# Performance work log

Hardware: AMD Instinct MI355X
Metric: run time of the kernel (lower is better)

Reference implementation:

```python
import jax, jax.numpy as jnp
import numpy as np

V, D, NL = 50257, 768, 12
DI, DS, DC, DTR = 1536, 16, 4, 48  # d_inner, d_state, d_conv, dt_rank
B, S = 2, 1024


def _mamba_layer(x, iw, cw, cb, xw, dw, db, Alog, Dp, ow):
    # x: (B,S,D)
    xz = x @ iw.T                      # (B,S,2*DI)
    xin, z = jnp.split(xz, 2, axis=-1)
    # depthwise causal conv over sequence
    xc = jax.lax.conv_general_dilated(
        jnp.transpose(xin, (0, 2, 1)), cw[:, None, :],
        window_strides=(1,), padding=[(DC - 1, 0)],
        feature_group_count=DI, dimension_numbers=('NCL', 'OIL', 'NCL'))
    xin = jax.nn.silu(jnp.transpose(xc, (0, 2, 1)) + cb)  # (B,S,DI)
    dbl = xin @ xw.T                   # (B,S,DTR+2*DS)
    dt, Bm, Cm = dbl[..., :DTR], dbl[..., DTR:DTR + DS], dbl[..., DTR + DS:]
    dt = jax.nn.softplus(dt @ dw.T + db)  # (B,S,DI)
    A = -jnp.exp(Alog)                 # (DI,DS)

    def step(h, inp):
        dt_t, B_t, C_t, x_t = inp      # (B,DI),(B,DS),(B,DS),(B,DI)
        h = h * jnp.exp(dt_t[:, :, None] * A) + (dt_t * x_t)[:, :, None] * B_t[:, None, :]
        y = jnp.einsum('bds,bs->bd', h, C_t)
        return h, y

    h0 = jnp.zeros((x.shape[0], DI, DS), dtype=x.dtype)
    xs = (jnp.transpose(dt, (1, 0, 2)), jnp.transpose(Bm, (1, 0, 2)),
          jnp.transpose(Cm, (1, 0, 2)), jnp.transpose(xin, (1, 0, 2)))
    _, ys = jax.lax.scan(step, h0, xs)
    y = jnp.transpose(ys, (1, 0, 2)) + xin * Dp  # (B,S,DI)
    y = y * jax.nn.silu(z)
    return y @ ow.T                    # (B,S,D)


def _layernorm(x, w, b):
    mu = jnp.mean(x, axis=-1, keepdims=True)
    var = jnp.mean(jnp.square(x - mu), axis=-1, keepdims=True)
    return (x - mu) * jax.lax.rsqrt(var + 1e-5) * w + b


def setup_inputs() -> dict:
    key = jax.random.key(0)
    ks = jax.random.split(key, 10)
    s = 0.02
    input_ids = jax.random.randint(ks[0], (B, S), 0, V)
    emb = jax.random.normal(ks[1], (V, D), jnp.float32) * s
    in_proj_w = jax.random.normal(ks[2], (NL, 2 * DI, D), jnp.float32) * s
    conv_w = jax.random.normal(ks[3], (NL, DI, DC), jnp.float32) * 0.2
    conv_b = jnp.zeros((NL, DI), jnp.float32)
    x_proj_w = jax.random.normal(ks[4], (NL, DTR + 2 * DS, DI), jnp.float32) * s
    dt_proj_w = jax.random.normal(ks[5], (NL, DI, DTR), jnp.float32) * (DTR ** -0.5)
    dt_proj_b = jax.random.normal(ks[6], (NL, DI), jnp.float32) * 0.1 - 4.0
    A_log = jnp.broadcast_to(jnp.log(jnp.arange(1, DS + 1, dtype=jnp.float32)), (NL, DI, DS)) + 0.0
    D_param = jnp.ones((NL, DI), jnp.float32)
    out_proj_w = jax.random.normal(ks[7], (NL, D, DI), jnp.float32) * s
    norm_w = jnp.ones((D,), jnp.float32)
    norm_b = jnp.zeros((D,), jnp.float32)
    return {"input_ids": input_ids, "emb": emb, "in_proj_w": in_proj_w,
            "conv_w": conv_w, "conv_b": conv_b, "x_proj_w": x_proj_w,
            "dt_proj_w": dt_proj_w, "dt_proj_b": dt_proj_b, "A_log": A_log,
            "D_param": D_param, "out_proj_w": out_proj_w,
            "norm_w": norm_w, "norm_b": norm_b}


def reference(input_ids, emb, in_proj_w, conv_w, conv_b, x_proj_w, dt_proj_w,
              dt_proj_b, A_log, D_param, out_proj_w, norm_w, norm_b):
    x = emb[input_ids] * (D ** 0.5)    # (B,S,D)
    for i in range(NL):
        x = _mamba_layer(x, in_proj_w[i], conv_w[i], conv_b[i], x_proj_w[i],
                         dt_proj_w[i], dt_proj_b[i], A_log[i], D_param[i], out_proj_w[i])
    x = _layernorm(x, norm_w, norm_b)
    return x @ emb.T                   # tied lm_head: (B,S,V)
```

## Files before the change

### kernel.cpp

```cpp
#include <hip/hip_runtime.h>
#include <hip/hip_bf16.h>

#define DI 1536
#define DS 16
#define DC 4
#define DTR 48
#define NB 2
#define SL 1024
#define DM 768
#define NLAYER 12
#define VOCAB 50257
#define ROWS (NB*SL)
#define CCH 32
#define CLEN (SL/CCH)
#define NBIG (DI+32)

typedef __attribute__((ext_vector_type(8))) short bf16x8;
typedef __attribute__((ext_vector_type(4))) short short4v;
typedef __attribute__((ext_vector_type(4))) float f32x4;

__device__ inline short f2bf(float f) {
    unsigned u = __builtin_bit_cast(unsigned, f);
    unsigned r = (u + 0x7fffu + ((u >> 16) & 1u)) >> 16;
    return (short)r;
}

__device__ __forceinline__ void gl_lds16(const void* g, void* l) {
    __builtin_amdgcn_global_load_lds(
        (const __attribute__((address_space(1))) unsigned int*)g,
        (__attribute__((address_space(3))) unsigned int*)l, 16, 0, 0);
}

__global__ __launch_bounds__(256) void cvt_bf16_k(const float* __restrict__ src,
                                                  unsigned short* __restrict__ dst,
                                                  int n4) {
    int i = blockIdx.x * 256 + threadIdx.x;
    if (i >= n4) return;
    float4 v = *reinterpret_cast<const float4*>(src + (size_t)i * 4);
    short4v o;
    o[0] = f2bf(v.x); o[1] = f2bf(v.y); o[2] = f2bf(v.z); o[3] = f2bf(v.w);
    *reinterpret_cast<short4v*>(dst + (size_t)i * 4) = o;
}

__global__ __launch_bounds__(256) void wc_k(
    const float* __restrict__ dtw_all,
    const float* __restrict__ xpw_all,
    unsigned short* __restrict__ wbig)
{
    int l = blockIdx.z;
    const float* dtw = dtw_all + (size_t)l * DI * DTR;
    const float* xpw = xpw_all + (size_t)l * 80 * DI;
    unsigned short* wb = wbig + (size_t)l * NBIG * DI;
    int tid = threadIdx.x;
    if (blockIdx.y == 12) {
        if (blockIdx.x == 0) {
            for (int idx = tid; idx < 32 * DI; idx += 256) {
                int rr = idx / DI, k = idx - rr * DI;
                wb[(size_t)(DI + rr) * DI + k] =
                    (unsigned short)f2bf(xpw[(size_t)(48 + rr) * DI + k]);
            }
        }
        return;
    }
    __shared__ float sd[128 * 48];
    __shared__ float sx[48 * 128];
    int d0 = blockIdx.y * 128, k0 = blockIdx.x * 128;
    for (int idx = tid; idx < 128 * 48; idx += 256) {
        int r = idx / 48, j = idx - r * 48;
        sd[idx] = dtw[(size_t)(d0 + r) * DTR + j];
    }
    for (int idx = tid; idx < 48 * 128; idx += 256) {
        int j = idx / 128, k = idx - j * 128;
        sx[idx] = xpw[(size_t)j * DI + k0 + k];
    }
    __syncthreads();
    int tx = tid & 15, ty = tid >> 4;
    float acc[8][8] = {};
    for (int j = 0; j < 48; ++j) {
        float a[8], w[8];
        #pragma unroll
        for (int i = 0; i < 8; ++i) a[i] = sd[(ty * 8 + i) * 48 + j];
        #pragma unroll
        for (int i = 0; i < 8; ++i) w[i] = sx[j * 128 + tx * 8 + i];
        #pragma unroll
        for (int i = 0; i < 8; ++i)
            #pragma unroll
            for (int jj = 0; jj < 8; ++jj)
                acc[i][jj] += a[i] * w[jj];
    }
    for (int i = 0; i < 8; ++i)
        for (int jj = 0; jj < 8; ++jj)
            wb[(size_t)(d0 + ty * 8 + i) * DI + k0 + tx * 8 + jj] =
                (unsigned short)f2bf(acc[i][jj]);
}

__global__ __launch_bounds__(256) void embed_k(const int* __restrict__ ids,
                                               const float* __restrict__ emb,
                                               unsigned short* __restrict__ xbf) {
    int i = blockIdx.x * 256 + threadIdx.x;
    if (i >= ROWS * DM) return;
    int row = i / DM;
    int c = i - row * DM;
    xbf[i] = (unsigned short)f2bf(emb[(size_t)ids[row] * DM + c] * 27.712812921102035f);
}

template<int MT, int OUT, bool NTST>
__global__ __launch_bounds__(256) void gemm_bf16(
    const unsigned short* __restrict__ A, int lda,
    const unsigned short* __restrict__ W, int ldw,
    float* __restrict__ C, unsigned short* __restrict__ Cbf, int ldc,
    int GY, int N, int K,
    const float* __restrict__ bias, float* __restrict__ aux)
{
    constexpr int BKT = 32;
    constexpr int CPR = BKT / 8;
    constexpr int ACA = MT * CPR / 256;
    constexpr int ACW = 128 * CPR / 256;
    constexpr int MFR = MT / 32;
    constexpr int BUFS = (MT + 128) * BKT;
    __shared__ __align__(16) short smem[2 * BUFS];

    const int tid  = threadIdx.x;
    const int lane = tid & 63;
    const int wid  = tid >> 6;
    const int wr   = wid >> 1, wc = wid & 1;

    const int nwg = gridDim.x;
    const int q = nwg >> 3, rm = nwg & 7;
    const int xcd = blockIdx.x & 7, bidx = blockIdx.x >> 3;
    const int wg = (xcd < rm ? xcd * (q + 1) : rm * (q + 1) + (xcd - rm) * q) + bidx;
    const int row0 = (wg % GY) * MT;
    const int col0 = (wg / GY) * 128;

    const unsigned short* gA[ACA];
    const unsigned short* gW[ACW];
    #pragma unroll
    for (int i = 0; i < ACA; ++i) {
        int cid = i * 256 + tid;
        int r = cid / CPR, c = cid % CPR;
        gA[i] = A + (size_t)(row0 + r) * lda + ((c ^ ((r >> 1) & 3)) * 8);
    }
    #pragma unroll
    for (int i = 0; i < ACW; ++i) {
        int cid = i * 256 + tid;
        int r = cid / CPR, c = cid % CPR;
        int rg = col0 + r; if (rg > N - 1) rg = N - 1;
        gW[i] = W + (size_t)rg * ldw + ((c ^ ((r >> 1) & 3)) * 8);
    }

    const int arow = wr * (MT / 2) + (lane & 15);
    const int brow = wc * 64 + (lane & 15);
    const int szA = (arow >> 1) & 3;
    const int szB = (brow >> 1) & 3;
    const int hi = lane >> 4;

    auto STAGE = [&](int buf) {
        short* As = smem + buf * BUFS;
        short* Ws = As + MT * BKT;
        #pragma unroll
        for (int i = 0; i < ACA; ++i) {
            gl_lds16(gA[i], &As[(i * 256 + wid * 64) * 8]);
            gA[i] += BKT;
        }
        #pragma unroll
        for (int i = 0; i < ACW; ++i) {
            gl_lds16(gW[i], &Ws[(i * 256 + wid * 64) * 8]);
            gW[i] += BKT;
        }
    };

    f32x4 acc[MFR][4] = {};

    STAGE(0);
    __syncthreads();

    const int ntiles = K / BKT;
    for (int t = 0; t < ntiles; ++t) {
        const int cur = t & 1;
        if (t + 1 < ntiles) STAGE(cur ^ 1);

        const short* As = smem + cur * BUFS;
        const short* Ws = As + MT * BKT;
        bf16x8 a[MFR], b[4];
        #pragma unroll
        for (int mf = 0; mf < MFR; ++mf)
            a[mf] = *reinterpret_cast<const bf16x8*>(
                &As[(arow + mf * 16) * BKT + ((hi ^ szA) * 8)]);
        #pragma unroll
        for (int nf = 0; nf < 4; ++nf)
            b[nf] = *reinterpret_cast<const bf16x8*>(
                &Ws[(brow + nf * 16) * BKT + ((hi ^ szB) * 8)]);
        #pragma unroll
        for (int mf = 0; mf < MFR; ++mf)
            #pragma unroll
            for (int nf = 0; nf < 4; ++nf)
                acc[mf][nf] = __builtin_amdgcn_mfma_f32_16x16x32_bf16(
                    a[mf], b[nf], acc[mf][nf], 0, 0, 0);

        __syncthreads();
    }

    if (OUT == 0 && NTST) {
        float* Cs = (float*)smem;
        #pragma unroll
        for (int mf = 0; mf < MFR; ++mf) {
            __syncthreads();
            #pragma unroll
            for (int nf = 0; nf < 4; ++nf) {
                #pragma unroll
                for (int j = 0; j < 4; ++j)
                    Cs[(wr * 16 + hi * 4 + j) * 132 + wc * 64 + nf * 16 + (lane & 15)]
                        = acc[mf][nf][j];
            }
            __syncthreads();
            #pragma unroll
            for (int rr = 0; rr < 8; ++rr) {
                int lrow = wid * 8 + rr;
                int grow = row0 + (lrow < 16 ? mf * 16 + lrow
                                             : (MT / 2) + mf * 16 + (lrow - 16));
                #pragma unroll
                for (int hf = 0; hf < 2; ++hf) {
                    int cc = col0 + hf * 64 + lane;
                    if (cc < N)
                        __builtin_nontemporal_store(
                            Cs[lrow * 132 + hf * 64 + lane],
                            &C[(size_t)grow * ldc + cc]);
                }
            }
        }
    } else {
        #pragma unroll
        for (int mf = 0; mf < MFR; ++mf) {
            #pragma unroll
            for (int nf = 0; nf < 4; ++nf) {
                int r  = row0 + wr * (MT / 2) + mf * 16 + hi * 4;
                int cc = col0 + wc * 64 + nf * 16 + (lane & 15);
                if (cc < N) {
                    f32x4 d = acc[mf][nf];
                    if (OUT == 3) {
                        if (cc < DI) {
                            float bv = bias[cc];
                            #pragma unroll
                            for (int j = 0; j < 4; ++j) {
                                float v = d[j] + bv;
                                v = (v > 20.f) ? v : log1pf(__expf(v));
                                C[(size_t)(r + j) * ldc + cc] = v;
                            }
                        } else {
                            #pragma unroll
                            for (int j = 0; j < 4; ++j)
                                aux[(size_t)(r + j) * 32 + (cc - DI)] = d[j];
                        }
                    } else {
                        #pragma unroll
                        for (int j = 0; j < 4; ++j) {
                            C[(size_t)(r + j) * ldc + cc] = d[j];
                            if (OUT == 1)
                                Cbf[(size_t)(r + j) * ldc + cc] =
                                    (unsigned short)f2bf(d[j]);
                        }
                    }
                }
            }
        }
    }
}

__global__ __launch_bounds__(256) void conv_silu_k(
    const float* __restrict__ xz, const float* __restrict__ cw,
    const float* __restrict__ cb, float* __restrict__ xinf,
    unsigned short* __restrict__ xinb)
{
    int i = blockIdx.x * 256 + threadIdx.x;
    if (i >= ROWS * DI) return;
    int row = i / DI;
    int c = i - row * DI;
    int t = row & (SL - 1);
    int b = row >> 10;
    float acc = cb[c];
    const float* base = xz + (size_t)(b * SL) * (2 * DI) + c;
    #pragma unroll
    for (int k = 0; k < DC; ++k) {
        int tt = t + k - (DC - 1);
        if (tt >= 0) acc += base[(size_t)tt * (2 * DI)] * cw[c * DC + k];
    }
    float v = acc / (1.f + __expf(-acc));
    xinf[i] = v;
    xinb[i] = (unsigned short)f2bf(v);
}

__global__ __launch_bounds__(256) void scan_phase1(
    const float* __restrict__ dt,
    const float* __restrict__ bc,
    const float* __restrict__ xin,
    const float* __restrict__ Alog,
    float* __restrict__ hend,
    float* __restrict__ eprod)
{
    int blk = blockIdx.x;
    int c = blk % CCH;
    int tmp = blk / CCH;
    int dblk = tmp % (DI / 16);
    int b = tmp / (DI / 16);
    int s = threadIdx.x & 15;
    int d = dblk * 16 + (threadIdx.x >> 4);
    float A = -__expf(Alog[d * DS + s]);
    float h = 0.f, P = 1.f;
    const int rowbase = b * SL + c * CLEN;
    #pragma unroll 4
    for (int t = 0; t < CLEN; ++t) {
        int r = rowbase + t;
        float dtv = dt[(size_t)r * DI + d];
        float xv  = xin[(size_t)r * DI + d];
        float Bv  = bc[(size_t)r * 32 + s];
        float e = __expf(dtv * A);
        h = h * e + dtv * xv * Bv;
        P *= e;
    }
    size_t idx = ((size_t)(b * CCH + c) * DI + d) * DS + s;
    hend[idx]  = h;
    eprod[idx] = P;
}

__global__ __launch_bounds__(256) void scan_phase3(
    const float* __restrict__ dt,
    const float* __restrict__ bc,
    const float* __restrict__ xin,
    const float* __restrict__ xz,
    const float* __restrict__ Alog,
    const float* __restrict__ Dp,
    const float* __restrict__ hend,
    const float* __restrict__ eprod,
    unsigned short* __restrict__ ybf)
{
    int blk = blockIdx.x;
    int c = blk % CCH;
    int tmp = blk / CCH;
    int dblk = tmp % (DI / 16);
    int b = tmp / (DI / 16);
    int s = threadIdx.x & 15;
    int d = dblk * 16 + (threadIdx.x >> 4);
    float A = -__expf(Alog[d * DS + s]);
    float Dv = Dp[d];

    float h = 0.f;
    const size_t pbase = ((size_t)b * CCH * DI + d) * DS + s;
    for (int j = 0; j < c; ++j) {
        size_t idx = pbase + (size_t)j * (DI * DS);
        h = h * eprod[idx] + hend[idx];
    }

    const int rowbase = b * SL + c * CLEN;
    #pragma unroll 2
    for (int t = 0; t < CLEN; ++t) {
        int r = rowbase + t;
        float dtv = dt[(size_t)r * DI + d];
        float xv  = xin[(size_t)r * DI + d];
        float Bv  = bc[(size_t)r * 32 + s];
        float Cv  = bc[(size_t)r * 32 + 16 + s];
        float e = __expf(dtv * A);
        h = h * e + dtv * xv * Bv;
        float p = h * Cv;
        p += __shfl_xor(p, 1, 64);
        p += __shfl_xor(p, 2, 64);
        p += __shfl_xor(p, 4, 64);
        p += __shfl_xor(p, 8, 64);
        if (s == 0) {
            float z = xz[(size_t)r * (2 * DI) + DI + d];
            float yv = (p + xv * Dv) * (z / (1.f + __expf(-z)));
            ybf[(size_t)r * DI + d] = (unsigned short)f2bf(yv);
        }
    }
}

__global__ __launch_bounds__(256) void ln_k(
    const float* __restrict__ x, const float* __restrict__ w,
    const float* __restrict__ b, unsigned short* __restrict__ o)
{
    int row = blockIdx.x;
    int tid = threadIdx.x;
    const float* xr = x + (size_t)row * DM;
    float v0 = xr[tid], v1 = xr[tid + 256], v2 = xr[tid + 512];
    float s = v0 + v1 + v2;
    #pragma unroll
    for (int off = 1; off < 64; off <<= 1) s += __shfl_xor(s, off, 64);
    __shared__ float red[4];
    __shared__ float red2[4];
    int wid = tid >> 6, lane = tid & 63;
    if (lane == 0) red[wid] = s;
    __syncthreads();
    float mu = (red[0] + red[1] + red[2] + red[3]) * (1.f / 768.f);
    float d0 = v0 - mu, d1 = v1 - mu, d2 = v2 - mu;
    float q = d0 * d0 + d1 * d1 + d2 * d2;
    #pragma unroll
    for (int off = 1; off < 64; off <<= 1) q += __shfl_xor(q, off, 64);
    if (lane == 0) red2[wid] = q;
    __syncthreads();
    float var = (red2[0] + red2[1] + red2[2] + red2[3]) * (1.f / 768.f);
    float rs = rsqrtf(var + 1e-5f);
    o[(size_t)row * DM + tid]       = (unsigned short)f2bf(d0 * rs * w[tid]       + b[tid]);
    o[(size_t)row * DM + tid + 256] = (unsigned short)f2bf(d1 * rs * w[tid + 256] + b[tid + 256]);
    o[(size_t)row * DM + tid + 512] = (unsigned short)f2bf(d2 * rs * w[tid + 512] + b[tid + 512]);
}

extern "C" void kernel_launch(void* const* d_in, const int* in_sizes, int n_in,
                              void* d_out, int out_size, void* d_ws, size_t ws_size,
                              hipStream_t stream) {
    const int*   ids        = (const int*)d_in[0];
    const float* emb        = (const float*)d_in[1];
    const float* in_proj_w  = (const float*)d_in[2];
    const float* conv_w     = (const float*)d_in[3];
    const float* conv_b     = (const float*)d_in[4];
    const float* x_proj_w   = (const float*)d_in[5];
    const float* dt_proj_w  = (const float*)d_in[6];
    const float* dt_proj_b  = (const float*)d_in[7];
    const float* A_log      = (const float*)d_in[8];
    const float* D_param    = (const float*)d_in[9];
    const float* out_proj_w = (const float*)d_in[10];
    const float* norm_w     = (const float*)d_in[11];
    const float* norm_b     = (const float*)d_in[12];
    float* out = (float*)d_out;

    char* base = (char*)d_ws;
    size_t off = 0;
    auto alloc_f = [&](size_t n) { float* p = (float*)(base + off); off += n * 4; return p; };
    auto alloc_u = [&](size_t n) { unsigned short* p = (unsigned short*)(base + off); off += n * 2; return p; };

    float* x     = alloc_f((size_t)ROWS * DM);
    float* xz    = alloc_f((size_t)ROWS * 2 * DI);
    float* xinf  = alloc_f((size_t)ROWS * DI);
    float* bc    = alloc_f((size_t)ROWS * 32);
    float* dt    = alloc_f((size_t)ROWS * DI);
    float* hend  = alloc_f((size_t)NB * CCH * DI * DS);
    float* eprod = alloc_f((size_t)NB * CCH * DI * DS);
    unsigned short* xbf   = alloc_u((size_t)ROWS * DM);
    unsigned short* ybf   = alloc_u((size_t)ROWS * DI);
    unsigned short* xinb  = alloc_u((size_t)ROWS * DI);
    unsigned short* xlnbf = alloc_u((size_t)ROWS * DM);
    unsigned short* inw_bf = alloc_u((size_t)NLAYER * 2 * DI * DM);
    unsigned short* ow_bf  = alloc_u((size_t)NLAYER * DM * DI);
    unsigned short* wbig  = alloc_u((size_t)NLAYER * NBIG * DI);
    unsigned short* emb_bf = alloc_u((size_t)VOCAB * DM);
    (void)ws_size;

    {
        int n4a = NLAYER * 2 * DI * DM / 4;
        cvt_bf16_k<<<(n4a + 255) / 256, 256, 0, stream>>>(in_proj_w, inw_bf, n4a);
        int n4b = NLAYER * DM * DI / 4;
        cvt_bf16_k<<<(n4b + 255) / 256, 256, 0, stream>>>(out_proj_w, ow_bf, n4b);
        wc_k<<<dim3(12, 13, NLAYER), 256, 0, stream>>>(dt_proj_w, x_proj_w, wbig);
        int n4e = VOCAB * DM / 4;
        cvt_bf16_k<<<(n4e + 255) / 256, 256, 0, stream>>>(emb, emb_bf, n4e);
    }

    embed_k<<<(ROWS * DM + 255) / 256, 256, 0, stream>>>(ids, emb, xbf);

    const int scan_grid = NB * (DI / 16) * CCH;

    for (int i = 0; i < NLAYER; ++i) {
        const float* cw  = conv_w  + (size_t)i * DI * DC;
        const float* cb  = conv_b  + (size_t)i * DI;
        const float* dtb = dt_proj_b + (size_t)i * DI;
        const float* Al  = A_log   + (size_t)i * DI * DS;
        const float* Dpar= D_param + (size_t)i * DI;

        const unsigned short* inw = inw_bf + (size_t)i * 2 * DI * DM;
        gemm_bf16<64, 0, false><<<24 * 32, 256, 0, stream>>>(
            xbf, DM, inw, DM, xz, nullptr, 2 * DI, 32, 2 * DI, DM, nullptr, nullptr);

        conv_silu_k<<<(ROWS * DI) / 256, 256, 0, stream>>>(xz, cw, cb, xinf, xinb);

        const unsigned short* wb = wbig + (size_t)i * NBIG * DI;
        gemm_bf16<64, 3, false><<<13 * 32, 256, 0, stream>>>(
            xinb, DI, wb, DI, dt, nullptr, DI, 32, NBIG, DI, dtb, bc);

        scan_phase1<<<scan_grid, 256, 0, stream>>>(dt, bc, xinf, Al, hend, eprod);
        scan_phase3<<<scan_grid, 256, 0, stream>>>(dt, bc, xinf, xz, Al, Dpar,
                                                   hend, eprod, ybf);

        const unsigned short* ow = ow_bf + (size_t)i * DM * DI;
        gemm_bf16<64, 1, false><<<6 * 32, 256, 0, stream>>>(
            ybf, DI, ow, DI, x, xbf, DM, 32, DM, DI, nullptr, nullptr);
    }

    ln_k<<<ROWS, 256, 0, stream>>>(x, norm_w, norm_b, xlnbf);
    gemm_bf16<128, 0, true><<<393 * 16, 256, 0, stream>>>(
        xlnbf, DM, emb_bf, DM, out, nullptr, VOCAB, 16, VOCAB, DM, nullptr, nullptr);
}
```

Measured before the change: 3.388 ms.

## Store intermediate activations in bf16 and use explicit vmcnt waits in GEMM

Intermediate activations (xz, conv output, dt, residual x) are now written and read as bf16 instead of fp32. This roughly halves the memory traffic in the conv, scan and layernorm kernels and removes the duplicate fp32 copies. The GEMM main loop also swaps __syncthreads for explicit s_waitcnt vmcnt plus raw s_barrier, so the next tile's async LDS loads can stay in flight while the current tile is computed. The cost is lower precision in the dt, x and z inputs to the scan and in the residual stream, which may move numerics closer to the tolerance.

```diff
diff --git a/kernel.cpp b/kernel.cpp
--- a/kernel.cpp
+++ b/kernel.cpp
@@ -24,6 +24,10 @@
     unsigned r = (u + 0x7fffu + ((u >> 16) & 1u)) >> 16;
     return (short)r;
 }
+__device__ inline float bf2f(unsigned short u) {
+    unsigned x = ((unsigned)u) << 16;
+    return __builtin_bit_cast(float, x);
+}
 
 __device__ __forceinline__ void gl_lds16(const void* g, void* l) {
     __builtin_amdgcn_global_load_lds(
@@ -116,6 +120,7 @@
     constexpr int CPR = BKT / 8;
     constexpr int ACA = MT * CPR / 256;
     constexpr int ACW = 128 * CPR / 256;
+    constexpr int ISS = ACA + ACW;
     constexpr int MFR = MT / 32;
     constexpr int BUFS = (MT + 128) * BKT;
     __shared__ __align__(16) short smem[2 * BUFS];
@@ -172,12 +177,17 @@
     f32x4 acc[MFR][4] = {};
 
     STAGE(0);
-    __syncthreads();
-
     const int ntiles = K / BKT;
     for (int t = 0; t < ntiles; ++t) {
         const int cur = t & 1;
-        if (t + 1 < ntiles) STAGE(cur ^ 1);
+        if (t + 1 < ntiles) {
+            STAGE(cur ^ 1);
+            asm volatile("s_waitcnt vmcnt(%0)" :: "n"(ISS) : "memory");
+        } else {
+            asm volatile("s_waitcnt vmcnt(0)" ::: "memory");
+        }
+        __builtin_amdgcn_sched_barrier(0);
+        __builtin_amdgcn_s_barrier();
 
         const short* As = smem + cur * BUFS;
         const short* Ws = As + MT * BKT;
@@ -197,10 +207,11 @@
                 acc[mf][nf] = __builtin_amdgcn_mfma_f32_16x16x32_bf16(
                     a[mf], b[nf], acc[mf][nf], 0, 0, 0);
 
+        __builtin_amdgcn_s_barrier();
+    }
+
+    if (OUT == 0 && NTST) {
         __syncthreads();
-    }
-
-    if (OUT == 0 && NTST) {
         float* Cs = (float*)smem;
         #pragma unroll
         for (int mf = 0; mf < MFR; ++mf) {
@@ -244,21 +255,21 @@
                             for (int j = 0; j < 4; ++j) {
                                 float v = d[j] + bv;
                                 v = (v > 20.f) ? v : log1pf(__expf(v));
-                                C[(size_t)(r + j) * ldc + cc] = v;
+                                Cbf[(size_t)(r + j) * ldc + cc] = (unsigned short)f2bf(v);
                             }
                         } else {
                             #pragma unroll
                             for (int j = 0; j < 4; ++j)
                                 aux[(size_t)(r + j) * 32 + (cc - DI)] = d[j];
                         }
+                    } else if (OUT == 2) {
+                        #pragma unroll
+                        for (int j = 0; j < 4; ++j)
+                            Cbf[(size_t)(r + j) * ldc + cc] = (unsigned short)f2bf(d[j]);
                     } else {
                         #pragma unroll
-                        for (int j = 0; j < 4; ++j) {
+                        for (int j = 0; j < 4; ++j)
                             C[(size_t)(r + j) * ldc + cc] = d[j];
-                            if (OUT == 1)
-                                Cbf[(size_t)(r + j) * ldc + cc] =
-                                    (unsigned short)f2bf(d[j]);
-                        }
                     }
                 }
             }
@@ -267,9 +278,8 @@
 }
 
 __global__ __launch_bounds__(256) void conv_silu_k(
-    const float* __restrict__ xz, const float* __restrict__ cw,
-    const float* __restrict__ cb, float* __restrict__ xinf,
-    unsigned short* __restrict__ xinb)
+    const unsigned short* __restrict__ xz, const float* __restrict__ cw,
+    const float* __restrict__ cb, unsigned short* __restrict__ xinb)
 {
     int i = blockIdx.x * 256 + threadIdx.x;
     if (i >= ROWS * DI) return;
@@ -278,21 +288,20 @@
     int t = row & (SL - 1);
     int b = row >> 10;
     float acc = cb[c];
-    const float* base = xz + (size_t)(b * SL) * (2 * DI) + c;
+    const unsigned short* base = xz + (size_t)(b * SL) * (2 * DI) + c;
     #pragma unroll
     for (int k = 0; k < DC; ++k) {
         int tt = t + k - (DC - 1);
-        if (tt >= 0) acc += base[(size_t)tt * (2 * DI)] * cw[c * DC + k];
+        if (tt >= 0) acc += bf2f(base[(size_t)tt * (2 * DI)]) * cw[c * DC + k];
     }
     float v = acc / (1.f + __expf(-acc));
-    xinf[i] = v;
     xinb[i] = (unsigned short)f2bf(v);
 }
 
 __global__ __launch_bounds__(256) void scan_phase1(
-    const float* __restrict__ dt,
+    const unsigned short* __restrict__ dt,
     const float* __restrict__ bc,
-    const float* __restrict__ xin,
+    const unsigned short* __restrict__ xin,
     const float* __restrict__ Alog,
     float* __restrict__ hend,
     float* __restrict__ eprod)
@@ -310,8 +319,8 @@
     #pragma unroll 4
     for (int t = 0; t < CLEN; ++t) {
         int r = rowbase + t;
-        float dtv = dt[(size_t)r * DI + d];
-        float xv  = xin[(size_t)r * DI + d];
+        float dtv = bf2f(dt[(size_t)r * DI + d]);
+        float xv  = bf2f(xin[(size_t)r * DI + d]);
         float Bv  = bc[(size_t)r * 32 + s];
         float e = __expf(dtv * A);
         h = h * e + dtv * xv * Bv;
@@ -323,10 +332,10 @@
 }
 
 __global__ __launch_bounds__(256) void scan_phase3(
-    const float* __restrict__ dt,
+    const unsigned short* __restrict__ dt,
     const float* __restrict__ bc,
-    const float* __restrict__ xin,
-    const float* __restrict__ xz,
+    const unsigned short* __restrict__ xin,
+    const unsigned short* __restrict__ xz,
     const float* __restrict__ Alog,
     const float* __restrict__ Dp,
     const float* __restrict__ hend,
@@ -354,8 +363,8 @@
     #pragma unroll 2
     for (int t = 0; t < CLEN; ++t) {
         int r = rowbase + t;
-        float dtv = dt[(size_t)r * DI + d];
-        float xv  = xin[(size_t)r * DI + d];
+        float dtv = bf2f(dt[(size_t)r * DI + d]);
+        float xv  = bf2f(xin[(size_t)r * DI + d]);
         float Bv  = bc[(size_t)r * 32 + s];
         float Cv  = bc[(size_t)r * 32 + 16 + s];
         float e = __expf(dtv * A);
@@ -366,7 +375,7 @@
         p += __shfl_xor(p, 4, 64);
         p += __shfl_xor(p, 8, 64);
         if (s == 0) {
-            float z = xz[(size_t)r * (2 * DI) + DI + d];
+            float z = bf2f(xz[(size_t)r * (2 * DI) + DI + d]);
             float yv = (p + xv * Dv) * (z / (1.f + __expf(-z)));
             ybf[(size_t)r * DI + d] = (unsigned short)f2bf(yv);
         }
@@ -374,13 +383,13 @@
 }
 
 __global__ __launch_bounds__(256) void ln_k(
-    const float* __restrict__ x, const float* __restrict__ w,
+    const unsigned short* __restrict__ x, const float* __restrict__ w,
     const float* __restrict__ b, unsigned short* __restrict__ o)
 {
     int row = blockIdx.x;
     int tid = threadIdx.x;
-    const float* xr = x + (size_t)row * DM;
-    float v0 = xr[tid], v1 = xr[tid + 256], v2 = xr[tid + 512];
+    const unsigned short* xr = x + (size_t)row * DM;
+    float v0 = bf2f(xr[tid]), v1 = bf2f(xr[tid + 256]), v2 = bf2f(xr[tid + 512]);
     float s = v0 + v1 + v2;
     #pragma unroll
     for (int off = 1; off < 64; off <<= 1) s += __shfl_xor(s, off, 64);
@@ -426,16 +435,14 @@
     auto alloc_f = [&](size_t n) { float* p = (float*)(base + off); off += n * 4; return p; };
     auto alloc_u = [&](size_t n) { unsigned short* p = (unsigned short*)(base + off); off += n * 2; return p; };
 
-    float* x     = alloc_f((size_t)ROWS * DM);
-    float* xz    = alloc_f((size_t)ROWS * 2 * DI);
-    float* xinf  = alloc_f((size_t)ROWS * DI);
     float* bc    = alloc_f((size_t)ROWS * 32);
-    float* dt    = alloc_f((size_t)ROWS * DI);
     float* hend  = alloc_f((size_t)NB * CCH * DI * DS);
     float* eprod = alloc_f((size_t)NB * CCH * DI * DS);
     unsigned short* xbf   = alloc_u((size_t)ROWS * DM);
+    unsigned short* xzb   = alloc_u((size_t)ROWS * 2 * DI);
+    unsigned short* xinb  = alloc_u((size_t)ROWS * DI);
+    unsigned short* dtbf  = alloc_u((size_t)ROWS * DI);
     unsigned short* ybf   = alloc_u((size_t)ROWS * DI);
-    unsigned short* xinb  = alloc_u((size_t)ROWS * DI);
     unsigned short* xlnbf = alloc_u((size_t)ROWS * DM);
     unsigned short* inw_bf = alloc_u((size_t)NLAYER * 2 * DI * DM);
     unsigned short* ow_bf  = alloc_u((size_t)NLAYER * DM * DI);
@@ -465,25 +472,25 @@
         const float* Dpar= D_param + (size_t)i * DI;
 
         const unsigned short* inw = inw_bf + (size_t)i * 2 * DI * DM;
-        gemm_bf16<64, 0, false><<<24 * 32, 256, 0, stream>>>(
-            xbf, DM, inw, DM, xz, nullptr, 2 * DI, 32, 2 * DI, DM, nullptr, nullptr);
-
-        conv_silu_k<<<(ROWS * DI) / 256, 256, 0, stream>>>(xz, cw, cb, xinf, xinb);
+        gemm_bf16<64, 2, false><<<24 * 32, 256, 0, stream>>>(
+            xbf, DM, inw, DM, nullptr, xzb, 2 * DI, 32, 2 * DI, DM, nullptr, nullptr);
+
+        conv_silu_k<<<(ROWS * DI) / 256, 256, 0, stream>>>(xzb, cw, cb, xinb);
 
         const unsigned short* wb = wbig + (size_t)i * NBIG * DI;
         gemm_bf16<64, 3, false><<<13 * 32, 256, 0, stream>>>(
-            xinb, DI, wb, DI, dt, nullptr, DI, 32, NBIG, DI, dtb, bc);
-
-        scan_phase1<<<scan_grid, 256, 0, stream>>>(dt, bc, xinf, Al, hend, eprod);
-        scan_phase3<<<scan_grid, 256, 0, stream>>>(dt, bc, xinf, xz, Al, Dpar,
+            xinb, DI, wb, DI, nullptr, dtbf, DI, 32, NBIG, DI, dtb, bc);
+
+        scan_phase1<<<scan_grid, 256, 0, stream>>>(dtbf, bc, xinb, Al, hend, eprod);
+        scan_phase3<<<scan_grid, 256, 0, stream>>>(dtbf, bc, xinb, xzb, Al, Dpar,
                                                    hend, eprod, ybf);
 
         const unsigned short* ow = ow_bf + (size_t)i * DM * DI;
-        gemm_bf16<64, 1, false><<<6 * 32, 256, 0, stream>>>(
-            ybf, DI, ow, DI, x, xbf, DM, 32, DM, DI, nullptr, nullptr);
-    }
-
-    ln_k<<<ROWS, 256, 0, stream>>>(x, norm_w, norm_b, xlnbf);
+        gemm_bf16<64, 2, false><<<6 * 32, 256, 0, stream>>>(
+            ybf, DI, ow, DI, nullptr, xbf, DM, 32, DM, DI, nullptr, nullptr);
+    }
+
+    ln_k<<<ROWS, 256, 0, stream>>>(xbf, norm_w, norm_b, xlnbf);
     gemm_bf16<128, 0, true><<<393 * 16, 256, 0, stream>>>(
         xlnbf, DM, emb_bf, DM, out, nullptr, VOCAB, 16, VOCAB, DM, nullptr, nullptr);
 }
```

New measurement: 3.204 ms. 5.4% less time.
